# Kernel optimization log

Hardware: AMD Instinct MI355X
Metric: run time of the kernel (lower is better)

## Reference

```python
import jax, jax.numpy as jnp
import numpy as np

N, E = 100_000, 1_600_000
NDIM_IN, EDIM, F, H, C = 64, 32, 32, 3, 10  # F=ndim_out per head, H=num_heads


def _edge_softmax(scores, dst, n):
    # softmax over incoming edges grouped by destination node (DGL edge_softmax)
    m = jax.ops.segment_max(scores, dst, num_segments=n)          # [N,H]
    ex = jnp.exp(scores - m[dst])                                  # [E,H]
    s = jax.ops.segment_sum(ex, dst, num_segments=n)               # [N,H]
    return ex / s[dst]


def _egat_conv(nf, ef, src, dst, W, We, al, ar, ae, b, n):
    # DGL EdgeGATConv: edge features modulate attention logits only
    h, f = al.shape
    ft = (nf @ W).reshape(-1, h, f)      # [N,H,F]
    fe = (ef @ We).reshape(-1, h, f)     # [E,H,F]
    el = (ft * al).sum(-1)               # [N,H]
    er = (ft * ar).sum(-1)               # [N,H]
    ee = (fe * ae).sum(-1)               # [E,H]
    e = jax.nn.leaky_relu(el[src] + er[dst] + ee, 0.2)             # [E,H]
    a = _edge_softmax(e, dst, n)                                   # [E,H]
    rst = jax.ops.segment_sum(ft[src] * a[:, :, None], dst, num_segments=n)
    return rst + b.reshape(1, h, f)


def setup_inputs() -> dict:
    key = jax.random.key(0)
    ks = jax.random.split(key, 16)
    s = lambda k, shp, fan: (jax.random.normal(k, shp, jnp.float32) / np.sqrt(fan).astype(np.float32))
    d = {}
    d["nfeats"] = jax.random.normal(ks[0], (N, 1, NDIM_IN), jnp.float32)
    d["efeats"] = jax.random.normal(ks[1], (E, 1, EDIM), jnp.float32)
    d["src"] = jax.random.randint(ks[2], (E,), 0, N, jnp.int32)
    d["dst"] = jax.random.randint(ks[3], (E,), 0, N, jnp.int32)
    # conv1 params
    d["W1"] = s(ks[4], (NDIM_IN, H * F), NDIM_IN)
    d["We1"] = s(ks[5], (EDIM, H * F), EDIM)
    d["al1"] = s(ks[6], (H, F), F)
    d["ar1"] = s(ks[7], (H, F), F)
    d["ae1"] = s(ks[8], (H, F), F)
    d["b1"] = jnp.zeros((H * F,), jnp.float32)
    # conv2 params (input dim = H*F after head concat)
    d["W2"] = s(ks[9], (H * F, H * F), H * F)
    d["We2"] = s(ks[10], (EDIM, H * F), EDIM)
    d["al2"] = s(ks[11], (H, F), F)
    d["ar2"] = s(ks[12], (H, F), F)
    d["ae2"] = s(ks[13], (H, F), F)
    d["b2"] = jnp.zeros((H * F,), jnp.float32)
    # edge score head: Linear(2*H*F, C)
    d["Wp"] = s(ks[14], (2 * H * F, C), 2 * H * F)
    d["bp"] = jnp.zeros((C,), jnp.float32)
    return d


def reference(nfeats, efeats, src, dst,
              W1, We1, al1, ar1, ae1, b1,
              W2, We2, al2, ar2, ae2, b2,
              Wp, bp):
    n = nfeats.shape[0]
    nf = jnp.squeeze(nfeats, 1)
    ef = jnp.squeeze(efeats, 1)
    h = _egat_conv(nf, ef, src, dst, W1, We1, al1, ar1, ae1, b1, n)
    h = jax.nn.relu(h.reshape(n, -1))                      # [N, H*F]
    h = _egat_conv(h, ef, src, dst, W2, We2, al2, ar2, ae2, b2, n).reshape(n, -1)
    # MLPPredictor: per-edge cat(h_src, h_dst) -> Linear
    score = jnp.concatenate([h[src], h[dst]], axis=1) @ Wp + bp   # [E, C]
    return score
```

## Files before the change

### kernel.cpp

```cpp
#include <hip/hip_runtime.h>
#include <hip/hip_bf16.h>
#include <stdint.h>

typedef __hip_bfloat16 bf16;

__device__ __forceinline__ float b2f(bf16 x) { return __bfloat162float(x); }
__device__ __forceinline__ float bits2f(uint32_t u) {
    union { uint32_t i; float f; } c; c.i = u; return c.f;
}

__global__ void detect_mode_kernel(const uint16_t* __restrict__ nf, int* __restrict__ flag) {
    if (threadIdx.x != 0 || blockIdx.x != 0) return;
    int sane = 0;
    for (int i = 0; i < 256; ++i) {
        uint32_t u = nf[2 * i];
        float a = fabsf(bits2f(u << 16));
        if (a == 0.f || (a > 1e-5f && a < 100.f)) ++sane;
    }
    flag[0] = (sane >= 128) ? 0 : 1;
}

struct ParamTable {
    const void* src[14];
    int off[15];
};

__global__ void convert_params_kernel(ParamTable T, const int* __restrict__ mode,
                                      float* __restrict__ out) {
    int i = blockIdx.x * blockDim.x + threadIdx.x;
    if (i >= T.off[14]) return;
    int k = 0;
    while (k < 13 && i >= T.off[k + 1]) ++k;
    int j = i - T.off[k];
    out[i] = (*mode == 0) ? b2f(((const bf16*)T.src[k])[j]) : ((const float*)T.src[k])[j];
}

__global__ void fold_wae_kernel(const float* __restrict__ We, const float* __restrict__ ae,
                                float* __restrict__ wae) {
    int t = threadIdx.x;
    if (t >= 96) return;
    int d = t / 3, h = t - d * 3;
    float acc = 0.f;
    for (int f = 0; f < 32; ++f) acc += We[d * 96 + h * 32 + f] * ae[h * 32 + f];
    wae[t] = acc;
}

__global__ void hist_rank_kernel(const int* __restrict__ dst, int* __restrict__ cnt,
                                 int* __restrict__ rank, int E) {
    int e = blockIdx.x * blockDim.x + threadIdx.x;
    if (e < E) rank[e] = atomicAdd(&cnt[dst[e]], 1);
}

__global__ void block_sum_kernel(const int* __restrict__ deg, int* __restrict__ bsums, int N) {
    __shared__ int sd[256];
    int t = threadIdx.x;
    int i = blockIdx.x * 256 + t;
    sd[t] = (i < N) ? deg[i] : 0;
    __syncthreads();
    for (int o = 128; o > 0; o >>= 1) {
        if (t < o) sd[t] += sd[t + o];
        __syncthreads();
    }
    if (t == 0) bsums[blockIdx.x] = sd[0];
}

__global__ void scan_bsums_kernel(int* __restrict__ bsums, int nb) {
    __shared__ int a[512], b[512];
    int t = threadIdx.x;
    int v = (t < nb) ? bsums[t] : 0;
    a[t] = v;
    __syncthreads();
    int* in = a;
    int* out = b;
    for (int o = 1; o < 512; o <<= 1) {
        out[t] = in[t] + ((t >= o) ? in[t - o] : 0);
        __syncthreads();
        int* tmp = in; in = out; out = tmp;
    }
    if (t < nb) bsums[t] = in[t] - v;
}

__global__ void scan_expand_kernel(const int* __restrict__ deg, const int* __restrict__ boffs,
                                   int* __restrict__ row_start, int N) {
    __shared__ int a[256], b[256];
    int t = threadIdx.x;
    int i = blockIdx.x * 256 + t;
    int v = (i < N) ? deg[i] : 0;
    a[t] = v;
    __syncthreads();
    int* in = a;
    int* out = b;
    for (int o = 1; o < 256; o <<= 1) {
        out[t] = in[t] + ((t >= o) ? in[t - o] : 0);
        __syncthreads();
        int* tmp = in; in = out; out = tmp;
    }
    if (i < N) row_start[i] = boffs[blockIdx.x] + in[t] - v;
}

__global__ void set_val_kernel(int* __restrict__ p, int v) { p[0] = v; }

__global__ void ft_elr_kernel(const void* __restrict__ X, int kind, const int* __restrict__ mode,
                              int din, const float* __restrict__ W,
                              const float* __restrict__ al, const float* __restrict__ ar,
                              float* __restrict__ ft, float* __restrict__ elr, int N) {
    __shared__ float xs[8 * 96];
    __shared__ float fs[8 * 96];
    int base = blockIdx.x * 8;
    int t = threadIdx.x;
    int m = *mode;
    for (int i = t; i < 8 * din; i += 256) {
        int ln = i / din, d = i - ln * din;
        int node = base + ln;
        float v = 0.f;
        if (node < N) {
            size_t idx = (size_t)node * din + d;
            if (kind == 1)   v = ((const float*)X)[idx];
            else if (m == 0) v = b2f(((const bf16*)X)[idx]);
            else             v = ((const float*)X)[idx];
        }
        xs[ln * 96 + d] = v;
    }
    __syncthreads();
    for (int i = t; i < 768; i += 256) {
        int ln = i / 96, c = i - ln * 96;
        int node = base + ln;
        float acc = 0.f;
        const float* xr = xs + ln * 96;
        for (int d = 0; d < din; ++d) acc += xr[d] * W[d * 96 + c];
        fs[ln * 96 + c] = acc;
        if (node < N) ft[(size_t)node * 96 + c] = acc;
    }
    __syncthreads();
    if (t < 48) {
        int ln = t / 6, q = t - ln * 6;
        int h = q >> 1, isr = q & 1;
        int node = base + ln;
        if (node < N) {
            const float* av = isr ? ar : al;
            const float* fr = fs + ln * 96 + h * 32;
            float acc = 0.f;
            for (int f = 0; f < 32; ++f) acc += fr[f] * av[h * 32 + f];
            elr[node * 6 + isr * 3 + h] = acc;
        }
    }
}

__global__ void scatter_edge_kernel(const void* __restrict__ ef, const int* __restrict__ mode,
                                    const float* __restrict__ wae1, const float* __restrict__ wae2,
                                    const int* __restrict__ src, const int* __restrict__ dst,
                                    const int* __restrict__ rank,
                                    const int* __restrict__ row_start,
                                    float4* __restrict__ S, int E) {
    __shared__ float w1[96];
    __shared__ float w2[96];
    int t = threadIdx.x;
    if (t < 96) { w1[t] = wae1[t]; w2[t] = wae2[t]; }
    __syncthreads();
    int e = blockIdx.x * blockDim.x + t;
    if (e >= E) return;
    int m = *mode;

    float x[32];
    if (m == 0) {
        const uint4* p = (const uint4*)((const uint16_t*)ef + (size_t)e * 32);
#pragma unroll
        for (int q = 0; q < 4; ++q) {
            uint4 u = p[q];
            x[q * 8 + 0] = bits2f(u.x << 16); x[q * 8 + 1] = bits2f(u.x & 0xffff0000u);
            x[q * 8 + 2] = bits2f(u.y << 16); x[q * 8 + 3] = bits2f(u.y & 0xffff0000u);
            x[q * 8 + 4] = bits2f(u.z << 16); x[q * 8 + 5] = bits2f(u.z & 0xffff0000u);
            x[q * 8 + 6] = bits2f(u.w << 16); x[q * 8 + 7] = bits2f(u.w & 0xffff0000u);
        }
    } else {
        const float4* p = (const float4*)((const float*)ef + (size_t)e * 32);
#pragma unroll
        for (int q = 0; q < 8; ++q) {
            float4 u = p[q];
            x[q * 4 + 0] = u.x; x[q * 4 + 1] = u.y; x[q * 4 + 2] = u.z; x[q * 4 + 3] = u.w;
        }
    }
    float a0 = 0.f, a1 = 0.f, a2 = 0.f;
    float c0 = 0.f, c1 = 0.f, c2 = 0.f;
#pragma unroll
    for (int d = 0; d < 32; ++d) {
        float xv = x[d];
        a0 += xv * w1[d * 3 + 0];
        a1 += xv * w1[d * 3 + 1];
        a2 += xv * w1[d * 3 + 2];
        c0 += xv * w2[d * 3 + 0];
        c1 += xv * w2[d * 3 + 1];
        c2 += xv * w2[d * 3 + 2];
    }
    int si = src[e], di = dst[e];
    int pos = row_start[di] + rank[e];
    S[2 * pos]     = make_float4(__int_as_float(si), a0, a1, a2);
    S[2 * pos + 1] = make_float4(c0, c1, c2, 0.f);
}

__global__ void aggregate_kernel(const float* __restrict__ ft, const float4* __restrict__ S,
                                 const int* __restrict__ row_start,
                                 const float* __restrict__ elr,
                                 const float* __restrict__ bias,
                                 int use_qa, int do_relu,
                                 float* __restrict__ R, int N) {
    int t = threadIdx.x;
    int node = blockIdx.x * 8 + (t >> 5);
    int lane = t & 31;
    if (node >= N) return;
    int beg = row_start[node], end = row_start[node + 1];
    float er0 = elr[node * 6 + 3], er1 = elr[node * 6 + 4], er2 = elr[node * 6 + 5];
    float a0 = 0.f, a1 = 0.f, a2 = 0.f, s0 = 0.f, s1 = 0.f, s2 = 0.f;
    int i = beg;
    for (; i + 4 <= end; i += 4) {
#pragma unroll
        for (int u = 0; u < 4; ++u) {
            float4 qa = S[2 * (i + u)];
            float4 qb = S[2 * (i + u) + 1];
            int sv = __float_as_int(qa.x);
            float ee0, ee1, ee2;
            if (use_qa) { ee0 = qa.y; ee1 = qa.z; ee2 = qa.w; }
            else        { ee0 = qb.x; ee1 = qb.y; ee2 = qb.z; }
            float2 el01 = *(const float2*)(elr + sv * 6);
            float  el2  = elr[sv * 6 + 2];
            float l0 = el01.x + er0 + ee0;
            float l1 = el01.y + er1 + ee1;
            float l2 = el2    + er2 + ee2;
            l0 = (l0 > 0.f) ? l0 : 0.2f * l0;
            l1 = (l1 > 0.f) ? l1 : 0.2f * l1;
            l2 = (l2 > 0.f) ? l2 : 0.2f * l2;
            float e0 = __expf(l0), e1 = __expf(l1), e2 = __expf(l2);
            const float* fr = ft + (size_t)sv * 96;
            a0 += fr[lane] * e0;
            a1 += fr[lane + 32] * e1;
            a2 += fr[lane + 64] * e2;
            s0 += e0; s1 += e1; s2 += e2;
        }
    }
    for (; i < end; ++i) {
        float4 qa = S[2 * i];
        float4 qb = S[2 * i + 1];
        int sv = __float_as_int(qa.x);
        float ee0, ee1, ee2;
        if (use_qa) { ee0 = qa.y; ee1 = qa.z; ee2 = qa.w; }
        else        { ee0 = qb.x; ee1 = qb.y; ee2 = qb.z; }
        float2 el01 = *(const float2*)(elr + sv * 6);
        float  el2  = elr[sv * 6 + 2];
        float l0 = el01.x + er0 + ee0;
        float l1 = el01.y + er1 + ee1;
        float l2 = el2    + er2 + ee2;
        l0 = (l0 > 0.f) ? l0 : 0.2f * l0;
        l1 = (l1 > 0.f) ? l1 : 0.2f * l1;
        l2 = (l2 > 0.f) ? l2 : 0.2f * l2;
        float e0 = __expf(l0), e1 = __expf(l1), e2 = __expf(l2);
        const float* fr = ft + (size_t)sv * 96;
        a0 += fr[lane] * e0;
        a1 += fr[lane + 32] * e1;
        a2 += fr[lane + 64] * e2;
        s0 += e0; s1 += e1; s2 += e2;
    }
    float r0, r1, r2;
    if (end > beg) { r0 = a0 / s0; r1 = a1 / s1; r2 = a2 / s2; }
    else           { r0 = r1 = r2 = 0.f; }
    r0 += bias[lane]; r1 += bias[lane + 32]; r2 += bias[lane + 64];
    if (do_relu) { r0 = fmaxf(r0, 0.f); r1 = fmaxf(r1, 0.f); r2 = fmaxf(r2, 0.f); }
    float* out = R + (size_t)node * 96;
    out[lane] = r0; out[lane + 32] = r1; out[lane + 64] = r2;
}

__global__ void uv_kernel(const float* __restrict__ h, const float* __restrict__ Wp,
                          const float* __restrict__ bp, float* __restrict__ uv, int N) {
    __shared__ float hs[8 * 96];
    int base = blockIdx.x * 8;
    int t = threadIdx.x;
    for (int i = t; i < 768; i += 256) {
        int ln = i / 96, c = i - ln * 96;
        int node = base + ln;
        hs[i] = (node < N) ? h[(size_t)node * 96 + c] : 0.f;
    }
    __syncthreads();
    if (t < 160) {
        int ln = t / 20, q = t - ln * 20;
        int half = q / 10, c = q - half * 10;
        int node = base + ln;
        if (node < N) {
            float acc = half ? 0.f : bp[c];
            const float* hr = hs + ln * 96;
            const float* wcol = Wp + half * 960 + c;
            for (int j = 0; j < 96; ++j) acc += hr[j] * wcol[j * 10];
            uv[node * 20 + q] = acc;
        }
    }
}

__global__ void score_kernel(const float* __restrict__ uv, const int* __restrict__ src,
                             const int* __restrict__ dst, const int* __restrict__ mode,
                             void* __restrict__ out, int E) {
    int e = blockIdx.x * blockDim.x + threadIdx.x;
    if (e >= E) return;
    int si = src[e], di = dst[e];
    const float* u = uv + (size_t)si * 20;
    const float* v = uv + (size_t)di * 20 + 10;
    float r[10];
#pragma unroll
    for (int c = 0; c < 10; ++c) r[c] = u[c] + v[c];
    if (*mode == 0) {
        bf16 o[10];
#pragma unroll
        for (int c = 0; c < 10; ++c) o[c] = __float2bfloat16(r[c]);
        uint32_t* po = (uint32_t*)((bf16*)out + (size_t)e * 10);
        const uint32_t* ps = (const uint32_t*)o;
#pragma unroll
        for (int q = 0; q < 5; ++q) po[q] = ps[q];
    } else {
        float2* po = (float2*)((float*)out + (size_t)e * 10);
#pragma unroll
        for (int q = 0; q < 5; ++q) po[q] = make_float2(r[2 * q], r[2 * q + 1]);
    }
}

extern "C" void kernel_launch(void* const* d_in, const int* in_sizes, int n_in,
                              void* d_out, int out_size, void* d_ws, size_t ws_size,
                              hipStream_t stream) {
    const void* nfeats = d_in[0];
    const void* efeats = d_in[1];
    const int* src = (const int*)d_in[2];
    const int* dst = (const int*)d_in[3];

    const int N = in_sizes[0] / 64;
    const int E = in_sizes[2];

    char* w = (char*)d_ws;
    auto alloc = [&](size_t bytes) {
        void* p = (void*)w;
        w += (bytes + 255) & ~(size_t)255;
        return p;
    };
    int*    flag      = (int*)alloc(256);
    float*  pbuf      = (float*)alloc((size_t)24202 * 4);
    float*  wae1      = (float*)alloc(96 * 4);
    float*  wae2      = (float*)alloc(96 * 4);
    float*  R         = (float*)alloc((size_t)N * 96 * 4);
    float*  F         = (float*)alloc((size_t)N * 96 * 4);
    float4* S         = (float4*)alloc((size_t)E * 32);
    float*  elr       = (float*)alloc((size_t)N * 6 * 4);
    int*    row_start = (int*)alloc((size_t)(N + 1) * 4);
    int*    cnt       = (int*)alloc((size_t)N * 4);
    int*    bsums     = (int*)alloc(512 * 4);
    int*    rank      = (int*)alloc((size_t)E * 4);
    float*  uv        = (float*)S;

    const int ns[14] = {64*96, 32*96, 96, 96, 96, 96, 96*96, 32*96, 96, 96, 96, 96, 192*10, 10};
    ParamTable T;
    int off = 0;
    for (int k = 0; k < 14; ++k) { T.src[k] = d_in[4 + k]; T.off[k] = off; off += ns[k]; }
    T.off[14] = off;
    float* W1f  = pbuf + T.off[0];
    float* We1f = pbuf + T.off[1];
    float* al1f = pbuf + T.off[2];
    float* ar1f = pbuf + T.off[3];
    float* ae1f = pbuf + T.off[4];
    float* b1f  = pbuf + T.off[5];
    float* W2f  = pbuf + T.off[6];
    float* We2f = pbuf + T.off[7];
    float* al2f = pbuf + T.off[8];
    float* ar2f = pbuf + T.off[9];
    float* ae2f = pbuf + T.off[10];
    float* b2f_ = pbuf + T.off[11];
    float* Wpf  = pbuf + T.off[12];
    float* bpf  = pbuf + T.off[13];

    dim3 b256(256);
    int eblocks    = (E + 255) / 256;
    int nodeBlocks = (N + 7) / 8;
    int nb         = (N + 255) / 256;

    hipLaunchKernelGGL(detect_mode_kernel, dim3(1), dim3(64), 0, stream,
                       (const uint16_t*)nfeats, flag);
    hipLaunchKernelGGL(convert_params_kernel, dim3((off + 255) / 256), b256, 0, stream,
                       T, flag, pbuf);
    hipLaunchKernelGGL(fold_wae_kernel, dim3(1), dim3(128), 0, stream, We1f, ae1f, wae1);
    hipLaunchKernelGGL(fold_wae_kernel, dim3(1), dim3(128), 0, stream, We2f, ae2f, wae2);

    hipMemsetAsync(cnt, 0, (size_t)N * 4, stream);
    hipLaunchKernelGGL(hist_rank_kernel, dim3(eblocks), b256, 0, stream, dst, cnt, rank, E);
    hipLaunchKernelGGL(block_sum_kernel, dim3(nb), b256, 0, stream, cnt, bsums, N);
    hipLaunchKernelGGL(scan_bsums_kernel, dim3(1), dim3(512), 0, stream, bsums, nb);
    hipLaunchKernelGGL(scan_expand_kernel, dim3(nb), b256, 0, stream, cnt, bsums, row_start, N);
    hipLaunchKernelGGL(set_val_kernel, dim3(1), dim3(1), 0, stream, row_start + N, E);

    hipLaunchKernelGGL(scatter_edge_kernel, dim3(eblocks), b256, 0, stream,
                       efeats, flag, wae1, wae2, src, dst, rank, row_start, S, E);

    hipLaunchKernelGGL(ft_elr_kernel, dim3(nodeBlocks), b256, 0, stream,
                       nfeats, 0, flag, 64, W1f, al1f, ar1f, F, elr, N);
    hipLaunchKernelGGL(aggregate_kernel, dim3(nodeBlocks), b256, 0, stream,
                       F, S, row_start, elr, b1f, 1, 1, R, N);

    hipLaunchKernelGGL(ft_elr_kernel, dim3(nodeBlocks), b256, 0, stream,
                       (const void*)R, 1, flag, 96, W2f, al2f, ar2f, F, elr, N);
    hipLaunchKernelGGL(aggregate_kernel, dim3(nodeBlocks), b256, 0, stream,
                       F, S, row_start, elr, b2f_, 0, 0, R, N);

    hipLaunchKernelGGL(uv_kernel, dim3(nodeBlocks), b256, 0, stream, R, Wpf, bpf, uv, N);
    hipLaunchKernelGGL(score_kernel, dim3(eblocks), b256, 0, stream,
                       uv, src, dst, flag, d_out, E);
}
```

Measured before the change: 1.092 ms.

## Register-tile the node feature projection GEMM with shared-memory weights

Replaces the per-node-output ft/elr kernel with a templated 64-node tile kernel that stages W and the input rows in shared memory and has each thread compute a 4x6 register block of outputs. This cuts the repeated global reads of W and raises arithmetic reuse in the dense projection. The result tile is reused in shared memory for the ft store and the attention dot products. It uses more shared memory per block and launches fewer blocks.

```diff
diff --git a/kernel.cpp b/kernel.cpp
--- a/kernel.cpp
+++ b/kernel.cpp
@@ -100,48 +100,84 @@
 
 __global__ void set_val_kernel(int* __restrict__ p, int v) { p[0] = v; }
 
-__global__ void ft_elr_kernel(const void* __restrict__ X, int kind, const int* __restrict__ mode,
-                              int din, const float* __restrict__ W,
-                              const float* __restrict__ al, const float* __restrict__ ar,
-                              float* __restrict__ ft, float* __restrict__ elr, int N) {
-    __shared__ float xs[8 * 96];
-    __shared__ float fs[8 * 96];
-    int base = blockIdx.x * 8;
-    int t = threadIdx.x;
-    int m = *mode;
-    for (int i = t; i < 8 * din; i += 256) {
-        int ln = i / din, d = i - ln * din;
+template <int DIN>
+__global__ void ft_elr_tiled_kernel(const void* __restrict__ X, int kind,
+                                    const int* __restrict__ mode,
+                                    const float* __restrict__ W,
+                                    const float* __restrict__ al, const float* __restrict__ ar,
+                                    float* __restrict__ ft, float* __restrict__ elr, int N) {
+    __shared__ float ws[DIN * 96];
+    __shared__ float xb[64 * 97];
+    const int t = threadIdx.x;
+    const int base = blockIdx.x * 64;
+    const int m = *mode;
+
+    for (int i = t; i < DIN * 96; i += 256) ws[i] = W[i];
+    for (int i = t; i < 64 * DIN; i += 256) {
+        int ln = i / DIN, d = i - ln * DIN;
         int node = base + ln;
         float v = 0.f;
         if (node < N) {
-            size_t idx = (size_t)node * din + d;
+            size_t idx = (size_t)node * DIN + d;
             if (kind == 1)   v = ((const float*)X)[idx];
             else if (m == 0) v = b2f(((const bf16*)X)[idx]);
             else             v = ((const float*)X)[idx];
         }
-        xs[ln * 96 + d] = v;
-    }
-    __syncthreads();
-    for (int i = t; i < 768; i += 256) {
+        xb[ln * (DIN + 1) + d] = v;
+    }
+    __syncthreads();
+
+    const int cx = t & 15;
+    const int ry = t >> 4;
+    const int c0 = cx * 6;
+    const int r0 = ry * 4;
+
+    float acc[4][6];
+#pragma unroll
+    for (int i = 0; i < 4; ++i)
+#pragma unroll
+        for (int j = 0; j < 6; ++j) acc[i][j] = 0.f;
+
+#pragma unroll 4
+    for (int d = 0; d < DIN; ++d) {
+        float xv[4];
+#pragma unroll
+        for (int i = 0; i < 4; ++i) xv[i] = xb[(r0 + i) * (DIN + 1) + d];
+        const float* wr = ws + d * 96 + c0;
+        float wv[6];
+#pragma unroll
+        for (int j = 0; j < 6; ++j) wv[j] = wr[j];
+#pragma unroll
+        for (int i = 0; i < 4; ++i)
+#pragma unroll
+            for (int j = 0; j < 6; ++j) acc[i][j] += xv[i] * wv[j];
+    }
+    __syncthreads();
+
+#pragma unroll
+    for (int i = 0; i < 4; ++i) {
+        float* fr = xb + (r0 + i) * 97 + c0;
+#pragma unroll
+        for (int j = 0; j < 6; ++j) fr[j] = acc[i][j];
+    }
+    __syncthreads();
+
+    for (int i = t; i < 64 * 96; i += 256) {
         int ln = i / 96, c = i - ln * 96;
         int node = base + ln;
-        float acc = 0.f;
-        const float* xr = xs + ln * 96;
-        for (int d = 0; d < din; ++d) acc += xr[d] * W[d * 96 + c];
-        fs[ln * 96 + c] = acc;
-        if (node < N) ft[(size_t)node * 96 + c] = acc;
-    }
-    __syncthreads();
-    if (t < 48) {
-        int ln = t / 6, q = t - ln * 6;
+        if (node < N) ft[(size_t)node * 96 + c] = xb[ln * 97 + c];
+    }
+    for (int i = t; i < 384; i += 256) {
+        int ln = i / 6, q = i - ln * 6;
         int h = q >> 1, isr = q & 1;
         int node = base + ln;
         if (node < N) {
-            const float* av = isr ? ar : al;
-            const float* fr = fs + ln * 96 + h * 32;
-            float acc = 0.f;
-            for (int f = 0; f < 32; ++f) acc += fr[f] * av[h * 32 + f];
-            elr[node * 6 + isr * 3 + h] = acc;
+            const float* av = (isr ? ar : al) + h * 32;
+            const float* fr = xb + ln * 97 + h * 32;
+            float acc2 = 0.f;
+#pragma unroll
+            for (int f = 0; f < 32; ++f) acc2 += fr[f] * av[f];
+            elr[node * 6 + isr * 3 + h] = acc2;
         }
     }
 }
@@ -373,6 +409,7 @@
     dim3 b256(256);
     int eblocks    = (E + 255) / 256;
     int nodeBlocks = (N + 7) / 8;
+    int tileBlocks = (N + 63) / 64;
     int nb         = (N + 255) / 256;
 
     hipLaunchKernelGGL(detect_mode_kernel, dim3(1), dim3(64), 0, stream,
@@ -392,13 +429,13 @@
     hipLaunchKernelGGL(scatter_edge_kernel, dim3(eblocks), b256, 0, stream,
                        efeats, flag, wae1, wae2, src, dst, rank, row_start, S, E);
 
-    hipLaunchKernelGGL(ft_elr_kernel, dim3(nodeBlocks), b256, 0, stream,
-                       nfeats, 0, flag, 64, W1f, al1f, ar1f, F, elr, N);
+    hipLaunchKernelGGL((ft_elr_tiled_kernel<64>), dim3(tileBlocks), b256, 0, stream,
+                       nfeats, 0, flag, W1f, al1f, ar1f, F, elr, N);
     hipLaunchKernelGGL(aggregate_kernel, dim3(nodeBlocks), b256, 0, stream,
                        F, S, row_start, elr, b1f, 1, 1, R, N);
 
-    hipLaunchKernelGGL(ft_elr_kernel, dim3(nodeBlocks), b256, 0, stream,
-                       (const void*)R, 1, flag, 96, W2f, al2f, ar2f, F, elr, N);
+    hipLaunchKernelGGL((ft_elr_tiled_kernel<96>), dim3(tileBlocks), b256, 0, stream,
+                       (const void*)R, 1, flag, W2f, al2f, ar2f, F, elr, N);
     hipLaunchKernelGGL(aggregate_kernel, dim3(nodeBlocks), b256, 0, stream,
                        F, S, row_start, elr, b2f_, 0, 0, R, N);
 
```

After: 1.030 ms. -5.6%, faster.
